# Performance work log

Measured on AMD Instinct MI355X. Metric: run time of the kernel, lower is better.

Reference implementation:

```python
import jax, jax.numpy as jnp
import numpy as np

B, S, D, H = 2, 2048, 1024, 16
HD = D // H  # 64
SCALE = float(np.sqrt(HD))


def setup_inputs() -> dict:
    key = jax.random.key(0)
    ks = jax.random.split(key, 5)
    x = jax.random.normal(ks[0], (B, S, D), dtype=jnp.float32)
    # causal mask: 1 = attend, 0 = masked
    mask = jnp.tril(jnp.ones((S, S), dtype=jnp.int32))
    xavier = lambda k: jax.random.normal(k, (D, D), dtype=jnp.float32) * np.sqrt(2.0 / (D + D))
    return {
        "x": x,
        "mask": mask,
        "Wq": xavier(ks[1]),
        "Wk": xavier(ks[2]),
        "Wv": xavier(ks[3]),
        "Wo": xavier(ks[4]),
    }


def reference(x, mask, Wq, Wk, Wv, Wo):
    # torch Linear(bias=False): y = x @ W.T  with W of shape [out, in]
    def heads(W):
        return (x @ W.T).reshape(B, S, H, HD).transpose(0, 2, 1, 3)  # [B,H,S,HD]

    Q, K, V = heads(Wq), heads(Wk), heads(Wv)
    scores = jnp.einsum("bhqd,bhkd->bhqk", Q, K) / SCALE  # [B,H,S,S]
    scores = jnp.where(mask[None, None] == 0, -jnp.inf, scores)
    attn = jax.nn.softmax(scores, axis=-1)
    attn = jnp.where(jnp.isnan(attn), jnp.zeros_like(attn), attn)  # nan-fix for fully masked rows
    # dropout is identity in eval / p=0
    out = jnp.einsum("bhqk,bhkd->bhqd", attn, V)  # [B,H,S,HD]
    out = out.transpose(0, 2, 1, 3).reshape(B, S, D)
    return out @ Wo.T
```

## Files before the change

### kernel.cpp

```cpp
#include <hip/hip_runtime.h>


using bfx8 = __attribute__((ext_vector_type(8))) short;
using bfx4 = __attribute__((ext_vector_type(4))) short;
using fx4  = __attribute__((ext_vector_type(4))) float;

#define NB 2
#define NS 2048
#define ND 1024
#define NH 16
#define NHD 64
#define LSTR 72

__device__ __forceinline__ unsigned short f2bf(float f) {
  union { float f; unsigned u; } v; v.f = f;
  return (unsigned short)((v.u + 0x7fffu + ((v.u >> 16) & 1u)) >> 16);
}
__device__ __forceinline__ unsigned pk2(float a, float b) {
  return (unsigned)f2bf(a) | ((unsigned)f2bf(b) << 16);
}
__device__ __forceinline__ unsigned pkt(float a, float b) {
  union { float f; unsigned u; } ua, ub; ua.f = a; ub.f = b;
  return (ua.u >> 16) | (ub.u & 0xffff0000u);
}

#define GLD16(gp, lp) __builtin_amdgcn_global_load_lds( \
    (__attribute__((address_space(1))) void*)(gp),      \
    (__attribute__((address_space(3))) void*)(lp), 16, 0, 0)

__global__ __launch_bounds__(256)
void cvt_all(const float4* __restrict__ x,  const float4* __restrict__ wq,
             const float4* __restrict__ wk, const float4* __restrict__ wv,
             const float4* __restrict__ wo, unsigned short* __restrict__ dst) {
  const int NT4 = (NB * NS * ND) / 4, NW4 = (ND * ND) / 4;
  const int i = blockIdx.x * 256 + threadIdx.x;
  const float4* src;
  int off;
  if (i < NT4) {
    src = x; off = i;
  } else {
    const int k = i - NT4;
    const int seg = k / NW4;
    off = k - seg * NW4;
    src = (seg == 0) ? wq : (seg == 1) ? wk : (seg == 2) ? wv : wo;
  }
  float4 f = src[off];
  uint2 w;
  w.x = pk2(f.x, f.y);
  w.y = pk2(f.z, f.w);
  *(uint2*)(dst + (size_t)i * 4) = w;
}

__global__ __launch_bounds__(256)
void gemm_qkvT(const unsigned short* __restrict__ Wcat,
               const unsigned short* __restrict__ xb,
               unsigned short* __restrict__ Qb, unsigned short* __restrict__ Kb,
               unsigned short* __restrict__ Vt, float SCL) {
  __shared__ __attribute__((aligned(16))) unsigned short As[128 * 32];
  __shared__ __attribute__((aligned(16))) unsigned short Bs[128 * 32];
  const int t = threadIdx.x;
  const int lane = t & 63, wave = t >> 6;
  const int wr = wave >> 1, wc = wave & 1;
  const int r16 = lane & 15, quad = lane >> 4;
  const int n0 = blockIdx.x * 128;
  const int m0 = blockIdx.y * 128;
  const int KD = 1024;
  fx4 acc[4][4] = {};
  const int c0 = t, c1 = t + 256;

  for (int k0 = 0; k0 < KD; k0 += 32) {
    GLD16(Wcat + (size_t)(n0 + (c0 >> 2)) * KD + (size_t)(c0 & 3) * 8 + k0, &As[c0 * 8]);
    GLD16(Wcat + (size_t)(n0 + (c1 >> 2)) * KD + (size_t)(c1 & 3) * 8 + k0, &As[c1 * 8]);
    GLD16(xb   + (size_t)(m0 + (c0 >> 2)) * KD + (size_t)(c0 & 3) * 8 + k0, &Bs[c0 * 8]);
    GLD16(xb   + (size_t)(m0 + (c1 >> 2)) * KD + (size_t)(c1 & 3) * 8 + k0, &Bs[c1 * 8]);
    __syncthreads();
    bfx8 af[4], bfr[4];
#pragma unroll
    for (int ni = 0; ni < 4; ni++)
      af[ni] = *(const bfx8*)&As[(wr * 64 + ni * 16 + r16) * 32 + quad * 8];
#pragma unroll
    for (int mi = 0; mi < 4; mi++)
      bfr[mi] = *(const bfx8*)&Bs[(wc * 64 + mi * 16 + r16) * 32 + quad * 8];
#pragma unroll
    for (int ni = 0; ni < 4; ni++)
#pragma unroll
      for (int mi = 0; mi < 4; mi++)
        acc[ni][mi] = __builtin_amdgcn_mfma_f32_16x16x32_bf16(
            af[ni], bfr[mi], acc[ni][mi], 0, 0, 0);
    __syncthreads();
  }
#pragma unroll
  for (int ni = 0; ni < 4; ni++) {
#pragma unroll
    for (int mi = 0; mi < 4; mi++) {
      fx4 v = acc[ni][mi];
      const int n = n0 + wr * 64 + ni * 16 + quad * 4;
      const int m = m0 + wc * 64 + mi * 16 + r16;
      const int b = m >> 11, s = m & (NS - 1);
      if (n0 < 1024) {
        const int h = n >> 6, hd = n & (NHD - 1);
        const size_t base = ((size_t)(b * NH + h) * NS + s) * NHD + hd;
        uint2 pw;
        pw.x = pk2(v[0] * SCL, v[1] * SCL);
        pw.y = pk2(v[2] * SCL, v[3] * SCL);
        *(uint2*)(Qb + base) = pw;
      } else if (n0 < 2048) {
        const int n2 = n - 1024;
        const int h = n2 >> 6, hd = n2 & (NHD - 1);
        const size_t base = ((size_t)(b * NH + h) * NS + s) * NHD + hd;
        uint2 pw;
        pw.x = pk2(v[0], v[1]);
        pw.y = pk2(v[2], v[3]);
        *(uint2*)(Kb + base) = pw;
      } else {
        const int n2 = n - 2048;
        const int h = n2 >> 6, hd = n2 & (NHD - 1);
        const size_t base = ((size_t)(b * NH + h) * NHD + hd) * NS + s;
#pragma unroll
        for (int r = 0; r < 4; r++) Vt[base + (size_t)r * NS] = f2bf(v[r]);
      }
    }
  }
}

__global__ __launch_bounds__(256)
void gemm_qkv_f32(const float* __restrict__ x,
                  const float* __restrict__ W0, const float* __restrict__ W1,
                  const float* __restrict__ W2,
                  unsigned short* __restrict__ Qb, unsigned short* __restrict__ Kb,
                  unsigned short* __restrict__ Vt, float SCL) {
  __shared__ __attribute__((aligned(16))) unsigned short As[128 * 32];
  __shared__ __attribute__((aligned(16))) unsigned short Bs[128 * 32];
  const int t = threadIdx.x;
  const int lane = t & 63, wave = t >> 6;
  const int wr = wave >> 1, wc = wave & 1;
  const int r16 = lane & 15, quad = lane >> 4;
  const int m0 = blockIdx.x * 128, n0 = blockIdx.y * 128;
  const int z = blockIdx.z;
  const float* W = (z == 0) ? W0 : (z == 1) ? W1 : W2;
  const int KD = 1024;
  fx4 acc[4][4] = {};
  const int row2 = t >> 1, kh = t & 1;
  for (int k0 = 0; k0 < KD; k0 += 32) {
    {
      const float4* src = (const float4*)(x + (size_t)(m0 + row2) * KD + k0 + kh * 16);
      float4 f0 = src[0], f1 = src[1], f2 = src[2], f3 = src[3];
      uint4 w0 = {pk2(f0.x, f0.y), pk2(f0.z, f0.w), pk2(f1.x, f1.y), pk2(f1.z, f1.w)};
      uint4 w1 = {pk2(f2.x, f2.y), pk2(f2.z, f2.w), pk2(f3.x, f3.y), pk2(f3.z, f3.w)};
      *(uint4*)&As[row2 * 32 + kh * 16] = w0;
      *(uint4*)&As[row2 * 32 + kh * 16 + 8] = w1;
    }
    {
      const float4* src = (const float4*)(W + (size_t)(n0 + row2) * KD + k0 + kh * 16);
      float4 f0 = src[0], f1 = src[1], f2 = src[2], f3 = src[3];
      uint4 w0 = {pk2(f0.x, f0.y), pk2(f0.z, f0.w), pk2(f1.x, f1.y), pk2(f1.z, f1.w)};
      uint4 w1 = {pk2(f2.x, f2.y), pk2(f2.z, f2.w), pk2(f3.x, f3.y), pk2(f3.z, f3.w)};
      *(uint4*)&Bs[row2 * 32 + kh * 16] = w0;
      *(uint4*)&Bs[row2 * 32 + kh * 16 + 8] = w1;
    }
    __syncthreads();
    bfx8 af[4], bfr[4];
#pragma unroll
    for (int mt = 0; mt < 4; mt++)
      af[mt] = *(const bfx8*)&As[(wr * 64 + mt * 16 + r16) * 32 + quad * 8];
#pragma unroll
    for (int nt = 0; nt < 4; nt++)
      bfr[nt] = *(const bfx8*)&Bs[(wc * 64 + nt * 16 + r16) * 32 + quad * 8];
#pragma unroll
    for (int mt = 0; mt < 4; mt++)
#pragma unroll
      for (int nt = 0; nt < 4; nt++)
        acc[mt][nt] = __builtin_amdgcn_mfma_f32_16x16x32_bf16(
            af[mt], bfr[nt], acc[mt][nt], 0, 0, 0);
    __syncthreads();
  }
#pragma unroll
  for (int mt = 0; mt < 4; mt++) {
#pragma unroll
    for (int nt = 0; nt < 4; nt++) {
      fx4 v = acc[mt][nt];
      const int mb = m0 + wr * 64 + mt * 16 + quad * 4;
      const int n = n0 + wc * 64 + nt * 16 + r16;
      const int b = mb >> 11, s = mb & (NS - 1);
      const int h = n >> 6, hd = n & (NHD - 1);
      if (z <= 1) {
        unsigned short* C = (z == 0) ? Qb : Kb;
        const float sc = (z == 0) ? SCL : 1.0f;
        const size_t base = ((size_t)(b * NH + h) * NS + s) * NHD + hd;
#pragma unroll
        for (int r = 0; r < 4; r++) C[base + (size_t)r * NHD] = f2bf(v[r] * sc);
      } else {
        const size_t base = ((size_t)(b * NH + h) * NHD + hd) * NS + s;
        uint2 pw;
        pw.x = pk2(v[0], v[1]);
        pw.y = pk2(v[2], v[3]);
        *(uint2*)(Vt + base) = pw;
      }
    }
  }
}

template <bool BF16>
__global__ __launch_bounds__(256)
void gemm_out(const unsigned short* __restrict__ A,
              const void* __restrict__ Wv,
              float* __restrict__ C) {
  __shared__ __attribute__((aligned(16))) unsigned short As[64 * 32];
  __shared__ __attribute__((aligned(16))) unsigned short Bs[128 * 32];
  const int t = threadIdx.x;
  const int lane = t & 63, wave = t >> 6;
  const int wr = wave >> 1, wc = wave & 1;
  const int r16 = lane & 15, quad = lane >> 4;
  const int m0 = blockIdx.x * 64, n0 = blockIdx.y * 128;
  const int KD = 1024;
  fx4 acc[2][4] = {};
  const int row2 = t >> 1, kh = t & 1;
  const int c0 = t, c1 = t + 256;
  for (int k0 = 0; k0 < KD; k0 += 32) {
    GLD16(A + (size_t)(m0 + (t >> 2)) * KD + (size_t)(t & 3) * 8 + k0, &As[t * 8]);
    if constexpr (BF16) {
      const unsigned short* W = (const unsigned short*)Wv;
      GLD16(W + (size_t)(n0 + (c0 >> 2)) * KD + (size_t)(c0 & 3) * 8 + k0, &Bs[c0 * 8]);
      GLD16(W + (size_t)(n0 + (c1 >> 2)) * KD + (size_t)(c1 & 3) * 8 + k0, &Bs[c1 * 8]);
    } else {
      const float* W = (const float*)Wv;
      const float4* src = (const float4*)(W + (size_t)(n0 + row2) * KD + k0 + kh * 16);
      float4 f0 = src[0], f1 = src[1], f2 = src[2], f3 = src[3];
      uint4 w0 = {pk2(f0.x, f0.y), pk2(f0.z, f0.w), pk2(f1.x, f1.y), pk2(f1.z, f1.w)};
      uint4 w1 = {pk2(f2.x, f2.y), pk2(f2.z, f2.w), pk2(f3.x, f3.y), pk2(f3.z, f3.w)};
      *(uint4*)&Bs[row2 * 32 + kh * 16] = w0;
      *(uint4*)&Bs[row2 * 32 + kh * 16 + 8] = w1;
    }
    __syncthreads();
    bfx8 af[2], bfr[4];
#pragma unroll
    for (int mt = 0; mt < 2; mt++)
      af[mt] = *(const bfx8*)&As[(wr * 32 + mt * 16 + r16) * 32 + quad * 8];
#pragma unroll
    for (int nt = 0; nt < 4; nt++)
      bfr[nt] = *(const bfx8*)&Bs[(wc * 64 + nt * 16 + r16) * 32 + quad * 8];
#pragma unroll
    for (int mt = 0; mt < 2; mt++)
#pragma unroll
      for (int nt = 0; nt < 4; nt++)
        acc[mt][nt] = __builtin_amdgcn_mfma_f32_16x16x32_bf16(
            af[mt], bfr[nt], acc[mt][nt], 0, 0, 0);
    __syncthreads();
  }
#pragma unroll
  for (int mt = 0; mt < 2; mt++) {
#pragma unroll
    for (int nt = 0; nt < 4; nt++) {
      fx4 v = acc[mt][nt];
      const int s = m0 + wr * 32 + mt * 16 + quad * 4;
      const int n = n0 + wc * 64 + nt * 16 + r16;
      const size_t base = (size_t)s * ND + n;
#pragma unroll
      for (int r = 0; r < 4; r++) C[base + (size_t)r * ND] = v[r];
    }
  }
}

__global__ __launch_bounds__(256)
void attn_mfma(const unsigned short* __restrict__ Q,
               const unsigned short* __restrict__ K,
               const unsigned short* __restrict__ Vt,
               unsigned short* __restrict__ O) {
  __shared__ __attribute__((aligned(16))) unsigned short Ks[64 * LSTR];
  __shared__ __attribute__((aligned(16))) unsigned short Vs[64 * LSTR];
  const int t = threadIdx.x;
  const int lane = t & 63, wave = t >> 6;
  const int r16 = lane & 15, quad = lane >> 4;
  const int bh = blockIdx.x;
  const int tile = 15 - blockIdx.y;
  const int b = bh >> 4, h = bh & (NH - 1);
  const int q0b = tile * 128;
  const int qbase = q0b + r16 * 8 + wave * 2;
  const int nT = (q0b + 128) >> 6;
  const unsigned short* Qp = Q + (size_t)bh * NS * NHD;
  const unsigned short* Kp = K + (size_t)bh * NS * NHD;
  const unsigned short* Vp = Vt + (size_t)bh * NHD * NS;

  bfx8 qf[2][2];
#pragma unroll
  for (int qt = 0; qt < 2; qt++)
#pragma unroll
    for (int hs = 0; hs < 2; hs++)
      qf[qt][hs] = *(const bfx8*)&Qp[(size_t)(qbase + qt) * NHD + hs * 32 + quad * 8];

  fx4 acc[2][4] = {};
  float lsum[2] = {0.0f, 0.0f};

  const int c0 = t, c1 = t + 256;
  uint4 kr0 = *(const uint4*)&Kp[8 * c0];
  uint4 kr1 = *(const uint4*)&Kp[8 * c1];
  uint4 vr0 = *(const uint4*)&Vp[(size_t)(c0 >> 3) * NS + (c0 & 7) * 8];
  uint4 vr1 = *(const uint4*)&Vp[(size_t)(c1 >> 3) * NS + (c1 & 7) * 8];

  for (int tt = 0; tt < nT; tt++) {
    __syncthreads();
    *(uint4*)&Ks[(c0 >> 3) * LSTR + (c0 & 7) * 8] = kr0;
    *(uint4*)&Ks[(c1 >> 3) * LSTR + (c1 & 7) * 8] = kr1;
    *(uint4*)&Vs[(c0 >> 3) * LSTR + (c0 & 7) * 8] = vr0;
    *(uint4*)&Vs[(c1 >> 3) * LSTR + (c1 & 7) * 8] = vr1;
    if (tt + 1 < nT) {
      const int kk = (tt + 1) * 64;
      kr0 = *(const uint4*)&Kp[kk * 64 + 8 * c0];
      kr1 = *(const uint4*)&Kp[kk * 64 + 8 * c1];
      vr0 = *(const uint4*)&Vp[(size_t)(c0 >> 3) * NS + kk + (c0 & 7) * 8];
      vr1 = *(const uint4*)&Vp[(size_t)(c1 >> 3) * NS + kk + (c1 & 7) * 8];
    }
    __syncthreads();

#pragma unroll
    for (int ks32 = 0; ks32 < 2; ks32++) {
      const int kkeff = tt * 64 + ks32 * 32;
      bfx8 kf[2][2];
      bfx4 vf[4][2];
#pragma unroll
      for (int kt = 0; kt < 2; kt++)
#pragma unroll
        for (int hs = 0; hs < 2; hs++)
          kf[kt][hs] = *(const bfx8*)&Ks[(ks32 * 32 + kt * 16 + r16) * LSTR + hs * 32 + quad * 8];
#pragma unroll
      for (int mt = 0; mt < 4; mt++)
#pragma unroll
        for (int ks = 0; ks < 2; ks++)
          vf[mt][ks] = *(const bfx4*)&Vs[(mt * 16 + r16) * LSTR + ks32 * 32 + ks * 16 + quad * 4];

      fx4 st[2][2] = {};
#pragma unroll
      for (int kt = 0; kt < 2; kt++)
#pragma unroll
        for (int qt = 0; qt < 2; qt++)
#pragma unroll
          for (int hs = 0; hs < 2; hs++)
            st[kt][qt] = __builtin_amdgcn_mfma_f32_16x16x32_bf16(
                kf[kt][hs], qf[qt][hs], st[kt][qt], 0, 0, 0);

      if (kkeff >= q0b) {
#pragma unroll
        for (int kt = 0; kt < 2; kt++)
#pragma unroll
          for (int qt = 0; qt < 2; qt++) {
            const int query = qbase + qt;
#pragma unroll
            for (int r = 0; r < 4; r++) {
              const int key = kkeff + kt * 16 + quad * 4 + r;
              if (key > query) st[kt][qt][r] = -1e30f;
            }
          }
      }

#pragma unroll
      for (int qt = 0; qt < 2; qt++) {
        float p[2][4];
        float ps = 0.0f;
#pragma unroll
        for (int kt = 0; kt < 2; kt++)
#pragma unroll
          for (int r = 0; r < 4; r++) {
            p[kt][r] = exp2f(st[kt][qt][r]);
            ps += p[kt][r];
          }
        lsum[qt] += ps;
        uint4 pbu;
        pbu.x = pkt(p[0][0], p[0][1]);
        pbu.y = pkt(p[0][2], p[0][3]);
        pbu.z = pkt(p[1][0], p[1][1]);
        pbu.w = pkt(p[1][2], p[1][3]);
        bfx8 pb = *(bfx8*)&pbu;
#pragma unroll
        for (int mt = 0; mt < 4; mt++) {
          bfx8 va = __builtin_shufflevector(vf[mt][0], vf[mt][1], 0, 1, 2, 3, 4, 5, 6, 7);
          acc[qt][mt] = __builtin_amdgcn_mfma_f32_16x16x32_bf16(
              va, pb, acc[qt][mt], 0, 0, 0);
        }
      }
    }
  }

#pragma unroll
  for (int qt = 0; qt < 2; qt++) {
    float l = lsum[qt];
    l += __shfl_xor(l, 16);
    l += __shfl_xor(l, 32);
    const float rinv = 1.0f / l;
    const int s = qbase + qt;
#pragma unroll
    for (int mt = 0; mt < 4; mt++) {
      const int d = h * NHD + mt * 16 + quad * 4;
      uint2 pw;
      pw.x = pk2(acc[qt][mt][0] * rinv, acc[qt][mt][1] * rinv);
      pw.y = pk2(acc[qt][mt][2] * rinv, acc[qt][mt][3] * rinv);
      *(uint2*)(O + ((size_t)b * NS + s) * ND + d) = pw;
    }
  }
}

extern "C" void kernel_launch(void* const* d_in, const int* in_sizes, int n_in,
                              void* d_out, int out_size, void* d_ws, size_t ws_size,
                              hipStream_t stream) {
  const float* x  = (const float*)d_in[0];
  const float* Wq = (const float*)d_in[2];
  const float* Wk = (const float*)d_in[3];
  const float* Wv = (const float*)d_in[4];
  const float* Wo = (const float*)d_in[5];
  float* out = (float*)d_out;
  unsigned short* ws = (unsigned short*)d_ws;
  const float QSCL = 0.125f * 1.44269504f;
  dim3 blk(256);
  const size_t NT = (size_t)NB * NS * ND;
  const size_t NW = (size_t)ND * ND;

  if (ws_size >= (size_t)48 * 1024 * 1024) {
    unsigned short* xb   = ws;
    unsigned short* Wcat = ws + NT;
    unsigned short* Wob  = ws + NT + 3 * NW;
    unsigned short* Qb   = ws + NT + 4 * NW;
    unsigned short* Kb   = Qb + NT;
    unsigned short* Vt   = Qb + 2 * NT;
    unsigned short* Ob   = Qb + 3 * NT;
    const int total4 = (int)((NT + 4 * NW) / 4);
    hipLaunchKernelGGL(cvt_all, dim3(total4 / 256), blk, 0, stream,
                       (const float4*)x, (const float4*)Wq, (const float4*)Wk,
                       (const float4*)Wv, (const float4*)Wo, xb);
    hipLaunchKernelGGL(gemm_qkvT, dim3(24, 32), blk, 0, stream,
                       Wcat, xb, Qb, Kb, Vt, QSCL);
    hipLaunchKernelGGL(attn_mfma, dim3(32, 16), blk, 0, stream, Qb, Kb, Vt, Ob);
    hipLaunchKernelGGL((gemm_out<true>), dim3(64, 8), blk, 0, stream, Ob, Wob, out);
  } else if (ws_size >= (size_t)32 * 1024 * 1024) {
    unsigned short* Qb = ws;
    unsigned short* Kb = ws + NT;
    unsigned short* Vt = ws + 2 * NT;
    unsigned short* Ob = ws + 3 * NT;
    hipLaunchKernelGGL(gemm_qkv_f32, dim3(32, 8, 3), blk, 0, stream,
                       x, Wq, Wk, Wv, Qb, Kb, Vt, QSCL);
    hipLaunchKernelGGL(attn_mfma, dim3(32, 16), blk, 0, stream, Qb, Kb, Vt, Ob);
    hipLaunchKernelGGL((gemm_out<false>), dim3(64, 8), blk, 0, stream, Ob, Wo, out);
  } else {
    const size_t NBA = (size_t)NS * ND;
    unsigned short* Qb = ws;
    unsigned short* Kb = ws + NBA;
    unsigned short* Vt = ws + 2 * NBA;
    unsigned short* Ob = ws + 3 * NBA;
    for (int b = 0; b < NB; b++) {
      const float* xb = x + (size_t)b * NS * ND;
      float* ob = out + (size_t)b * NS * ND;
      hipLaunchKernelGGL(gemm_qkv_f32, dim3(16, 8, 3), blk, 0, stream,
                         xb, Wq, Wk, Wv, Qb, Kb, Vt, QSCL);
      hipLaunchKernelGGL(attn_mfma, dim3(16, 16), blk, 0, stream, Qb, Kb, Vt, Ob);
      hipLaunchKernelGGL((gemm_out<false>), dim3(32, 8), blk, 0, stream, Ob, Wo, ob);
    }
  }
}
```

Before: 192.6 us.

## Shrink attention query tile to 64 rows and add MFMA wave priority

```diff
diff --git a/kernel.cpp b/kernel.cpp
--- a/kernel.cpp
+++ b/kernel.cpp
@@ -272,24 +272,22 @@
   const int lane = t & 63, wave = t >> 6;
   const int r16 = lane & 15, quad = lane >> 4;
   const int bh = blockIdx.x;
-  const int tile = 15 - blockIdx.y;
+  const int tile = 31 - blockIdx.y;
   const int b = bh >> 4, h = bh & (NH - 1);
-  const int q0b = tile * 128;
-  const int qbase = q0b + r16 * 8 + wave * 2;
-  const int nT = (q0b + 128) >> 6;
+  const int q0b = tile * 64;
+  const int qbase = q0b + r16 * 4 + wave;
+  const int nT = tile + 1;
   const unsigned short* Qp = Q + (size_t)bh * NS * NHD;
   const unsigned short* Kp = K + (size_t)bh * NS * NHD;
   const unsigned short* Vp = Vt + (size_t)bh * NHD * NS;
 
-  bfx8 qf[2][2];
-#pragma unroll
-  for (int qt = 0; qt < 2; qt++)
-#pragma unroll
-    for (int hs = 0; hs < 2; hs++)
-      qf[qt][hs] = *(const bfx8*)&Qp[(size_t)(qbase + qt) * NHD + hs * 32 + quad * 8];
-
-  fx4 acc[2][4] = {};
-  float lsum[2] = {0.0f, 0.0f};
+  bfx8 qf[2];
+#pragma unroll
+  for (int hs = 0; hs < 2; hs++)
+    qf[hs] = *(const bfx8*)&Qp[(size_t)qbase * NHD + hs * 32 + quad * 8];
+
+  fx4 acc[4] = {};
+  float lsum = 0.0f;
 
   const int c0 = t, c1 = t + 256;
   uint4 kr0 = *(const uint4*)&Kp[8 * c0];
@@ -328,71 +326,65 @@
         for (int ks = 0; ks < 2; ks++)
           vf[mt][ks] = *(const bfx4*)&Vs[(mt * 16 + r16) * LSTR + ks32 * 32 + ks * 16 + quad * 4];
 
-      fx4 st[2][2] = {};
+      fx4 st[2] = {};
+      __builtin_amdgcn_s_setprio(1);
 #pragma unroll
       for (int kt = 0; kt < 2; kt++)
 #pragma unroll
-        for (int qt = 0; qt < 2; qt++)
-#pragma unroll
-          for (int hs = 0; hs < 2; hs++)
-            st[kt][qt] = __builtin_amdgcn_mfma_f32_16x16x32_bf16(
-                kf[kt][hs], qf[qt][hs], st[kt][qt], 0, 0, 0);
+        for (int hs = 0; hs < 2; hs++)
+          st[kt] = __builtin_amdgcn_mfma_f32_16x16x32_bf16(
+              kf[kt][hs], qf[hs], st[kt], 0, 0, 0);
+      __builtin_amdgcn_s_setprio(0);
 
       if (kkeff >= q0b) {
 #pragma unroll
         for (int kt = 0; kt < 2; kt++)
 #pragma unroll
-          for (int qt = 0; qt < 2; qt++) {
-            const int query = qbase + qt;
-#pragma unroll
-            for (int r = 0; r < 4; r++) {
-              const int key = kkeff + kt * 16 + quad * 4 + r;
-              if (key > query) st[kt][qt][r] = -1e30f;
-            }
+          for (int r = 0; r < 4; r++) {
+            const int key = kkeff + kt * 16 + quad * 4 + r;
+            if (key > qbase) st[kt][r] = -1e30f;
           }
       }
 
-#pragma unroll
-      for (int qt = 0; qt < 2; qt++) {
-        float p[2][4];
-        float ps = 0.0f;
-#pragma unroll
-        for (int kt = 0; kt < 2; kt++)
-#pragma unroll
-          for (int r = 0; r < 4; r++) {
-            p[kt][r] = exp2f(st[kt][qt][r]);
-            ps += p[kt][r];
-          }
-        lsum[qt] += ps;
-        uint4 pbu;
-        pbu.x = pkt(p[0][0], p[0][1]);
-        pbu.y = pkt(p[0][2], p[0][3]);
-        pbu.z = pkt(p[1][0], p[1][1]);
-        pbu.w = pkt(p[1][2], p[1][3]);
-        bfx8 pb = *(bfx8*)&pbu;
-#pragma unroll
-        for (int mt = 0; mt < 4; mt++) {
-          bfx8 va = __builtin_shufflevector(vf[mt][0], vf[mt][1], 0, 1, 2, 3, 4, 5, 6, 7);
-          acc[qt][mt] = __builtin_amdgcn_mfma_f32_16x16x32_bf16(
-              va, pb, acc[qt][mt], 0, 0, 0);
+      float p[2][4];
+      float ps = 0.0f;
+#pragma unroll
+      for (int kt = 0; kt < 2; kt++)
+#pragma unroll
+        for (int r = 0; r < 4; r++) {
+          p[kt][r] = exp2f(st[kt][r]);
+          ps += p[kt][r];
         }
+      lsum += ps;
+      uint4 pbu;
+      pbu.x = pkt(p[0][0], p[0][1]);
+      pbu.y = pkt(p[0][2], p[0][3]);
+      pbu.z = pkt(p[1][0], p[1][1]);
+      pbu.w = pkt(p[1][2], p[1][3]);
+      bfx8 pb = *(bfx8*)&pbu;
+      __builtin_amdgcn_s_setprio(1);
+#pragma unroll
+      for (int mt = 0; mt < 4; mt++) {
+        bfx8 va = __builtin_shufflevector(vf[mt][0], vf[mt][1], 0, 1, 2, 3, 4, 5, 6, 7);
+        acc[mt] = __builtin_amdgcn_mfma_f32_16x16x32_bf16(
+            va, pb, acc[mt], 0, 0, 0);
       }
-    }
-  }
-
-#pragma unroll
-  for (int qt = 0; qt < 2; qt++) {
-    float l = lsum[qt];
+      __builtin_amdgcn_s_setprio(0);
+    }
+  }
+
+  {
+    float l = lsum;
     l += __shfl_xor(l, 16);
     l += __shfl_xor(l, 32);
     const float rinv = 1.0f / l;
-    const int s = qbase + qt;
+    const int s = qbase;
 #pragma unroll
     for (int mt = 0; mt < 4; mt++) {
       const int d = h * NHD + mt * 16 + quad * 4;
       uint2 pw;
-      pw.x = pk2(acc[qt][mt][0] * rinv, acc[qt][mt][1] * rinv);
-      pw.y = pk2(acc[qt][mt][2] * rinv, acc[qt][mt][3] * rinv);
+      pw.x = pk2(acc[mt][0] * rinv, acc[mt][1] * rinv);
+      pw.y = pk2(acc[mt][2] * rinv, acc[mt][3] * rinv);
       *(uint2*)(O + ((size_t)b * NS + s) * ND + d) = pw;
     }
   }
@@ -427,7 +419,7 @@
                        (const float4*)Wv, (const float4*)Wo, xb);
     hipLaunchKernelGGL(gemm_qkvT, dim3(24, 32), blk, 0, stream,
                        Wcat, xb, Qb, Kb, Vt, QSCL);
-    hipLaunchKernelGGL(attn_mfma, dim3(32, 16), blk, 0, stream, Qb, Kb, Vt, Ob);
+    hipLaunchKernelGGL(attn_mfma, dim3(32, 32), blk, 0, stream, Qb, Kb, Vt, Ob);
     hipLaunchKernelGGL((gemm_out<true>), dim3(64, 8), blk, 0, stream, Ob, Wob, out);
   } else if (ws_size >= (size_t)32 * 1024 * 1024) {
     unsigned short* Qb = ws;
@@ -436,7 +428,7 @@
     unsigned short* Ob = ws + 3 * NT;
     hipLaunchKernelGGL(gemm_qkv_f32, dim3(32, 8, 3), blk, 0, stream,
                        x, Wq, Wk, Wv, Qb, Kb, Vt, QSCL);
-    hipLaunchKernelGGL(attn_mfma, dim3(32, 16), blk, 0, stream, Qb, Kb, Vt, Ob);
+    hipLaunchKernelGGL(attn_mfma, dim3(32, 32), blk, 0, stream, Qb, Kb, Vt, Ob);
     hipLaunchKernelGGL((gemm_out<false>), dim3(64, 8), blk, 0, stream, Ob, Wo, out);
   } else {
     const size_t NBA = (size_t)NS * ND;
@@ -449,7 +441,7 @@
       float* ob = out + (size_t)b * NS * ND;
       hipLaunchKernelGGL(gemm_qkv_f32, dim3(16, 8, 3), blk, 0, stream,
                          xb, Wq, Wk, Wv, Qb, Kb, Vt, QSCL);
-      hipLaunchKernelGGL(attn_mfma, dim3(16, 16), blk, 0, stream, Qb, Kb, Vt, Ob);
+      hipLaunchKernelGGL(attn_mfma, dim3(16, 32), blk, 0, stream, Qb, Kb, Vt, Ob);
       hipLaunchKernelGGL((gemm_out<false>), dim3(32, 8), blk, 0, stream, Ob, Wo, ob);
     }
   }
```

After: 188.8 us. -2.0%, faster.
